# Performance work log

Measured on AMD Instinct MI355X. Metric: run time of the kernel, lower is better.

Reference implementation:

```python
import jax, jax.numpy as jnp
import numpy as np

TEMPERATURE = 1.0
NEG = -1e9
EPS = 1e-8


def setup_inputs() -> dict:
    key = jax.random.key(0)
    k1, k2, k3 = jax.random.split(key, 3)
    B, H = 524288, 32
    scores = jax.random.normal(k1, (B, H), dtype=jnp.float32)
    rankings = jax.random.randint(k2, (B, H), 0, 33, dtype=jnp.int32)
    mask = jax.random.randint(k3, (B, H), 0, 2, dtype=jnp.int32).astype(bool)
    return {"scores": scores, "rankings": rankings, "mask": mask}


def reference(scores, rankings, mask):
    B, H = scores.shape
    # effective validity: horse present AND has a ranking > 0 (top_k=None)
    m = mask & (rankings > 0)
    # masked, temperature-scaled scores; -1e9 entries underflow to exactly 0 in softmax
    s = jnp.where(m, scores / TEMPERATURE, NEG)
    p = jax.nn.softmax(s, axis=1)  # [B, H], ~0 at invalid slots

    n_valid = jnp.sum(m, axis=1)  # [B]
    # ideal order: valid horses sorted by ranking ascending (invalid pushed to end)
    rank_key = jnp.where(m, rankings, jnp.iinfo(jnp.int32).max)
    rank_order = jnp.argsort(rank_key, axis=1)          # stable sort
    # prediction order: valid horses in original index order (matches torch.where)
    pos_order = jnp.argsort(~m, axis=1)                 # stable: valid first

    q = jnp.take_along_axis(p, rank_order, axis=1)      # ideal_probs, aligned by list position
    pr = jnp.take_along_axis(p, pos_order, axis=1)      # pred_probs,  aligned by list position

    # positions >= n_valid are padding
    valid_pos = jnp.arange(H)[None, :] < n_valid[:, None]
    q_safe = jnp.where(valid_pos, q, 1.0)
    pr_safe = jnp.where(valid_pos, pr, 1.0)
    # KL(ideal || pred) with the original's log(pred + 1e-8)
    kl_terms = q_safe * (jnp.log(q_safe) - jnp.log(pr_safe + EPS))
    kl = jnp.sum(jnp.where(valid_pos, kl_terms, 0.0), axis=1)  # [B]

    # rows with <= 1 valid ranked horse are skipped entirely
    row_ok = n_valid > 1
    n_rows = jnp.maximum(jnp.sum(row_ok), 1)
    return jnp.sum(jnp.where(row_ok, kl, 0.0)) / n_rows  # reduction='mean'
```

## Files before the change

kernel.cpp:

```cpp
#include <hip/hip_runtime.h>
#include <stdint.h>


#define H 32
#define BLK 256
#define WPB 4
#define ROWD 17
#define WREGION (64 * ROWD)

__global__ __launch_bounds__(BLK) void listwise_kernel(
    const float* __restrict__ scores,
    const int* __restrict__ rankings,
    const unsigned char* __restrict__ mask_u8,
    float* __restrict__ part_kl,
    float* __restrict__ part_cnt,
    int nrows)
{
    __shared__ uint32_t stage[WPB * WREGION];
    __shared__ float s_kl[WPB], s_cnt[WPB];

    const int tid  = threadIdx.x;
    const int lane = tid & 63;
    const int wid  = tid >> 6;
    uint32_t* wbuf = &stage[wid * WREGION];
    const int wrow0 = blockIdx.x * BLK + wid * 64;

    float kl = 0.0f, cnt = 0.0f;
    uint32_t kp[16], sw[16];
    int nv = 0;
    bool have_row = false;
    unsigned short* rowp = (unsigned short*)&wbuf[lane * ROWD];

    const bool full = (wrow0 + 64 <= nrows);

    uint4 pr[8], ps[8];
    uint32_t pmw[8];
    if (full) {
        const uint4* r4 = (const uint4*)(rankings + (size_t)wrow0 * H);
        const uint4* s4 = (const uint4*)(scores + (size_t)wrow0 * H);
        const uint32_t* m1 = (const uint32_t*)(mask_u8 + (size_t)wrow0 * H);
        #pragma unroll
        for (int c = 0; c < 8; ++c) pr[c] = r4[lane + 64 * c];
        #pragma unroll
        for (int c = 0; c < 8; ++c) ps[c] = s4[lane + 64 * c];
        #pragma unroll
        for (int c = 0; c < 8; ++c) pmw[c] = m1[lane + 64 * c];
    }

    unsigned char probe = mask_u8[lane];
    const bool mask_is_i32 =
        (__ballot(((lane & 3) != 0) && (probe != 0)) == 0ull);

    if (full) {
        have_row = true;

        #pragma unroll
        for (int c = 0; c < 8; ++c) {
            const uint4 v = ps[c];
            const int L = (lane + 64 * c) << 2;
            uint32_t* d = &wbuf[(L >> 5) * ROWD + ((L & 31) >> 1)];
            d[0] = ((v.x + 0x8000u) >> 16) | (((v.y + 0x8000u) >> 16) << 16);
            d[1] = ((v.z + 0x8000u) >> 16) | (((v.w + 0x8000u) >> 16) << 16);
        }
        {
            const uint32_t* rb = &wbuf[lane * ROWD];
            #pragma unroll
            for (int a = 0; a < 16; ++a) sw[a] = rb[a];
        }

        if (!mask_is_i32) {
            #pragma unroll
            for (int c = 0; c < 8; ++c) {
                const uint4 rv = pr[c];
                const uint32_t mv = pmw[c];
                const int L = (lane + 64 * c) << 2;
                const uint32_t t0 = ((mv & 0x000000FFu) != 0u && (int)rv.x > 0) ? (rv.x << 5) : 0x4000u;
                const uint32_t t1 = ((mv & 0x0000FF00u) != 0u && (int)rv.y > 0) ? (rv.y << 5) : 0x4000u;
                const uint32_t t2 = ((mv & 0x00FF0000u) != 0u && (int)rv.z > 0) ? (rv.z << 5) : 0x4000u;
                const uint32_t t3 = ((mv & 0xFF000000u) != 0u && (int)rv.w > 0) ? (rv.w << 5) : 0x4000u;
                uint32_t* d = &wbuf[(L >> 5) * ROWD + ((L & 31) >> 1)];
                d[0] = t0 | (t1 << 16);
                d[1] = t2 | (t3 << 16);
            }
        } else {
            const uint4* m4 =
                (const uint4*)((const uint32_t*)mask_u8 + (size_t)wrow0 * H);
            #pragma unroll
            for (int c = 0; c < 8; ++c) {
                const uint4 rv = pr[c];
                const uint4 mv = m4[lane + 64 * c];
                const int L = (lane + 64 * c) << 2;
                const uint32_t t0 = (mv.x != 0u && (int)rv.x > 0) ? (rv.x << 5) : 0x4000u;
                const uint32_t t1 = (mv.y != 0u && (int)rv.y > 0) ? (rv.y << 5) : 0x4000u;
                const uint32_t t2 = (mv.z != 0u && (int)rv.z > 0) ? (rv.z << 5) : 0x4000u;
                const uint32_t t3 = (mv.w != 0u && (int)rv.w > 0) ? (rv.w << 5) : 0x4000u;
                uint32_t* d = &wbuf[(L >> 5) * ROWD + ((L & 31) >> 1)];
                d[0] = t0 | (t1 << 16);
                d[1] = t2 | (t3 << 16);
            }
        }
        {
            const uint32_t* rb = &wbuf[lane * ROWD];
            uint32_t inv2 = 0;
            #pragma unroll
            for (int a = 0; a < 16; ++a) {
                const uint32_t w = rb[a];
                kp[a] = w | ((uint32_t)(2 * a) | (((uint32_t)(2 * a + 1)) << 16));
                inv2 += (w >> 14) & 0x00010001u;
            }
            nv = 32 - (int)((inv2 & 0xFFFFu) + (inv2 >> 16));
        }
        {
            int jp = 0;
            #pragma unroll
            for (int a = 0; a < 16; ++a) {
                const uint32_t s2 = sw[a];
                const uint32_t kw = kp[a];
                const bool v0 = (kw & 0xFFFFu) < 0x4000u;
                const bool v1 = (kw >> 16) < 0x4000u;
                rowp[v0 ? jp : 33] = (unsigned short)(s2 & 0xFFFFu);
                jp += v0 ? 1 : 0;
                rowp[v1 ? jp : 33] = (unsigned short)(s2 >> 16);
                jp += v1 ? 1 : 0;
            }
        }
    } else if (wrow0 + lane < nrows) {
        have_row = true;
        const int row = wrow0 + lane;
        const int*   rptr = rankings + (size_t)row * H;
        const float* sptr = scores + (size_t)row * H;
        uint32_t vbits = 0;
        if (mask_is_i32) {
            const int* mp = (const int*)mask_u8 + (size_t)row * H;
            #pragma unroll
            for (int k = 0; k < H; ++k) vbits |= (mp[k] != 0 ? 1u : 0u) << k;
        } else {
            const unsigned char* mp = mask_u8 + (size_t)row * H;
            #pragma unroll
            for (int k = 0; k < H; ++k) vbits |= (mp[k] != 0 ? 1u : 0u) << k;
        }
        int jp = 0;
        #pragma unroll
        for (int a = 0; a < 16; ++a) {
            uint32_t kq[2], bq[2];
            #pragma unroll
            for (int q = 0; q < 2; ++q) {
                const int k = 2 * a + q;
                const int r = rptr[k];
                const bool valid = (((vbits >> k) & 1u) != 0u) && (r > 0);
                kq[q] = valid ? ((((uint32_t)r) << 5) | (uint32_t)k)
                              : (0x4000u | (uint32_t)k);
                nv += valid ? 1 : 0;
                bq[q] = (__float_as_uint(sptr[k]) + 0x8000u) >> 16;
                rowp[valid ? jp : 33] = (unsigned short)bq[q];
                jp += valid ? 1 : 0;
            }
            kp[a] = kq[0] | (kq[1] << 16);
            sw[a] = bq[0] | (bq[1] << 16);
        }
    }

    if (have_row) {
        uint32_t w32[32];
        #pragma unroll
        for (int a = 0; a < 16; ++a) {
            const uint32_t kw = kp[a], s2 = sw[a];
            w32[2 * a]     = (kw << 16) | (s2 & 0xFFFFu);
            w32[2 * a + 1] = (kw & 0xFFFF0000u) | (s2 >> 16);
        }
        #pragma unroll
        for (int k = 2; k <= 32; k <<= 1) {
            #pragma unroll
            for (int j = k >> 1; j > 0; j >>= 1) {
                #pragma unroll
                for (int i = 0; i < 32; ++i) {
                    const int l = i ^ j;
                    if (l > i) {
                        const uint32_t a = w32[i], b = w32[l];
                        const uint32_t mn = a < b ? a : b;
                        const uint32_t mx = a < b ? b : a;
                        const bool up = ((i & k) == 0);
                        w32[i] = up ? mn : mx;
                        w32[l] = up ? mx : mn;
                    }
                }
            }
        }

        float se = 0.0f, num = 0.0f;
        const uint32_t* rbd = &wbuf[lane * ROWD];
        #pragma unroll
        for (int a = 0; a < 16; ++a) {
            const uint32_t cw = rbd[a];
            #pragma unroll
            for (int q = 0; q < 2; ++q) {
                const uint32_t wv = w32[2 * a + q];
                const bool valid = wv < 0x40000000u;
                const float s_i = __uint_as_float(wv << 16);
                const uint32_t c16 = q ? (cw >> 16) : (cw & 0xFFFFu);
                const float g = __uint_as_float(c16 << 16);
                float e = __expf(s_i);
                e = valid ? e : 0.0f;
                const float d2 = valid ? (s_i - g) : 0.0f;
                se += e;
                num = __builtin_fmaf(e, d2, num);
            }
        }
        if (nv > 1) { kl = __fdividef(num, se); cnt = 1.0f; }
    }

    #pragma unroll
    for (int m = 32; m >= 1; m >>= 1) {
        kl  += __shfl_xor(kl, m);
        cnt += __shfl_xor(cnt, m);
    }
    if (lane == 0) { s_kl[wid] = kl; s_cnt[wid] = cnt; }
    __syncthreads();
    if (tid == 0) {
        part_kl[blockIdx.x]  = s_kl[0] + s_kl[1] + s_kl[2] + s_kl[3];
        part_cnt[blockIdx.x] = s_cnt[0] + s_cnt[1] + s_cnt[2] + s_cnt[3];
    }
}

__global__ __launch_bounds__(256) void finalize_kernel(
    const float* __restrict__ part_kl,
    const float* __restrict__ part_cnt,
    float* __restrict__ out, int nblk)
{
    float k = 0.0f, c = 0.0f;
    for (int i = threadIdx.x; i < nblk; i += 256) {
        k += part_kl[i];
        c += part_cnt[i];
    }
    #pragma unroll
    for (int m = 32; m >= 1; m >>= 1) {
        k += __shfl_xor(k, m);
        c += __shfl_xor(c, m);
    }
    __shared__ float sk[4], sc[4];
    const int wid = threadIdx.x >> 6;
    if ((threadIdx.x & 63) == 0) { sk[wid] = k; sc[wid] = c; }
    __syncthreads();
    if (threadIdx.x == 0) {
        float K = sk[0] + sk[1] + sk[2] + sk[3];
        float C = sc[0] + sc[1] + sc[2] + sc[3];
        if (C < 1.0f) C = 1.0f;
        out[0] = K / C;
    }
}

extern "C" void kernel_launch(void* const* d_in, const int* in_sizes, int n_in,
                              void* d_out, int out_size, void* d_ws, size_t ws_size,
                              hipStream_t stream) {
    const float* scores = (const float*)d_in[0];
    const int* rankings = (const int*)d_in[1];
    const unsigned char* mask = (const unsigned char*)d_in[2];
    float* out = (float*)d_out;

    const int total = in_sizes[0];
    const int nrows = total / H;
    const int blocks = (nrows + BLK - 1) / BLK;

    float* part_kl  = (float*)d_ws;
    float* part_cnt = (float*)d_ws + blocks;

    listwise_kernel<<<blocks, BLK, 0, stream>>>(
        scores, rankings, mask, part_kl, part_cnt, nrows);

    finalize_kernel<<<1, 256, 0, stream>>>(part_kl, part_cnt, out, blocks);
}
```

Baseline: 199.7 us.

## Rewrite as persistent single-wave blocks with double-buffered global-to-LDS loads

Replaces the 256-thread blocks with 64-thread persistent blocks (about 1024 of them), each looping over several 64-row tiles. Rankings, scores and the u8 mask are copied straight into LDS with global_load_lds, double-buffered so the next tile's load overlaps compute on the current one. Instead of compacting valid scores through LDS, each row now builds two key arrays and sorts both with a bitonic network: one ordered by ranking, one by original index. This is meant to hide memory latency and cut LDS round trips, at the cost of a second sort per row, fewer waves in flight, and a full vmcnt(0) wait per tile.

```diff
diff --git a/kernel.cpp b/kernel.cpp
--- a/kernel.cpp
+++ b/kernel.cpp
@@ -3,210 +3,225 @@
 
 
 #define H 32
-#define BLK 256
-#define WPB 4
-#define ROWD 17
-#define WREGION (64 * ROWD)
-
-__global__ __launch_bounds__(BLK) void listwise_kernel(
+#define TPB 64
+#define RANK_DW 2048
+#define SCORE_DW 2048
+#define MASK_DW 512
+#define BUF_DW (RANK_DW + SCORE_DW + MASK_DW)
+
+__device__ __forceinline__ void glds16(const void* g, void* l) {
+    __builtin_amdgcn_global_load_lds(
+        (const __attribute__((address_space(1))) void*)g,
+        (__attribute__((address_space(3))) void*)l, 16, 0, 0);
+}
+
+__device__ __forceinline__ void sort32(uint32_t* w) {
+    #pragma unroll
+    for (int k = 2; k <= 32; k <<= 1) {
+        #pragma unroll
+        for (int j = k >> 1; j > 0; j >>= 1) {
+            #pragma unroll
+            for (int i = 0; i < 32; ++i) {
+                const int l = i ^ j;
+                if (l > i) {
+                    const uint32_t a = w[i], b = w[l];
+                    const uint32_t mn = a < b ? a : b;
+                    const uint32_t mx = a < b ? b : a;
+                    const bool up = ((i & k) == 0);
+                    w[i] = up ? mn : mx;
+                    w[l] = up ? mx : mn;
+                }
+            }
+        }
+    }
+}
+
+__global__ __launch_bounds__(TPB) void listwise_kernel(
     const float* __restrict__ scores,
     const int* __restrict__ rankings,
     const unsigned char* __restrict__ mask_u8,
     float* __restrict__ part_kl,
     float* __restrict__ part_cnt,
-    int nrows)
+    int nrows, int tpw)
 {
-    __shared__ uint32_t stage[WPB * WREGION];
-    __shared__ float s_kl[WPB], s_cnt[WPB];
-
-    const int tid  = threadIdx.x;
-    const int lane = tid & 63;
-    const int wid  = tid >> 6;
-    uint32_t* wbuf = &stage[wid * WREGION];
-    const int wrow0 = blockIdx.x * BLK + wid * 64;
-
-    float kl = 0.0f, cnt = 0.0f;
-    uint32_t kp[16], sw[16];
-    int nv = 0;
-    bool have_row = false;
-    unsigned short* rowp = (unsigned short*)&wbuf[lane * ROWD];
-
-    const bool full = (wrow0 + 64 <= nrows);
-
-    uint4 pr[8], ps[8];
-    uint32_t pmw[8];
-    if (full) {
-        const uint4* r4 = (const uint4*)(rankings + (size_t)wrow0 * H);
-        const uint4* s4 = (const uint4*)(scores + (size_t)wrow0 * H);
-        const uint32_t* m1 = (const uint32_t*)(mask_u8 + (size_t)wrow0 * H);
-        #pragma unroll
-        for (int c = 0; c < 8; ++c) pr[c] = r4[lane + 64 * c];
-        #pragma unroll
-        for (int c = 0; c < 8; ++c) ps[c] = s4[lane + 64 * c];
-        #pragma unroll
-        for (int c = 0; c < 8; ++c) pmw[c] = m1[lane + 64 * c];
-    }
+    __shared__ __align__(16) uint32_t buf[2][BUF_DW];
+
+    const int lane  = threadIdx.x;
+    const int tile0 = blockIdx.x * tpw;
 
     unsigned char probe = mask_u8[lane];
+    {
+        const int r0 = tile0 * 64;
+        if (r0 + 64 <= nrows) {
+            const char* rb = (const char*)(rankings + (size_t)r0 * H);
+            const char* sb = (const char*)(scores + (size_t)r0 * H);
+            #pragma unroll
+            for (int c = 0; c < 8; ++c)
+                glds16(rb + c * 1024 + lane * 16, &buf[0][c * 256]);
+            #pragma unroll
+            for (int c = 0; c < 8; ++c)
+                glds16(sb + c * 1024 + lane * 16, &buf[0][RANK_DW + c * 256]);
+        }
+    }
     const bool mask_is_i32 =
         (__ballot(((lane & 3) != 0) && (probe != 0)) == 0ull);
-
-    if (full) {
-        have_row = true;
-
-        #pragma unroll
-        for (int c = 0; c < 8; ++c) {
-            const uint4 v = ps[c];
-            const int L = (lane + 64 * c) << 2;
-            uint32_t* d = &wbuf[(L >> 5) * ROWD + ((L & 31) >> 1)];
-            d[0] = ((v.x + 0x8000u) >> 16) | (((v.y + 0x8000u) >> 16) << 16);
-            d[1] = ((v.z + 0x8000u) >> 16) | (((v.w + 0x8000u) >> 16) << 16);
-        }
+    {
+        const int r0 = tile0 * 64;
+        if (!mask_is_i32 && r0 + 64 <= nrows) {
+            const char* mb = (const char*)(mask_u8 + (size_t)r0 * H);
+            #pragma unroll
+            for (int c = 0; c < 2; ++c)
+                glds16(mb + c * 1024 + lane * 16,
+                       &buf[0][RANK_DW + SCORE_DW + c * 256]);
+        }
+    }
+
+    float kl = 0.0f, cnt = 0.0f;
+    int cur = 0;
+
+    for (int tt = 0; tt < tpw; ++tt) {
+        const int row0 = (tile0 + tt) * 64;
+        if (row0 >= nrows) break;
+        const bool full = (row0 + 64 <= nrows);
+
+        if (full) {
+            asm volatile("s_waitcnt vmcnt(0)" ::: "memory");
+            __builtin_amdgcn_sched_barrier(0);
+        }
+
         {
-            const uint32_t* rb = &wbuf[lane * ROWD];
-            #pragma unroll
-            for (int a = 0; a < 16; ++a) sw[a] = rb[a];
-        }
-
-        if (!mask_is_i32) {
-            #pragma unroll
-            for (int c = 0; c < 8; ++c) {
-                const uint4 rv = pr[c];
-                const uint32_t mv = pmw[c];
-                const int L = (lane + 64 * c) << 2;
-                const uint32_t t0 = ((mv & 0x000000FFu) != 0u && (int)rv.x > 0) ? (rv.x << 5) : 0x4000u;
-                const uint32_t t1 = ((mv & 0x0000FF00u) != 0u && (int)rv.y > 0) ? (rv.y << 5) : 0x4000u;
-                const uint32_t t2 = ((mv & 0x00FF0000u) != 0u && (int)rv.z > 0) ? (rv.z << 5) : 0x4000u;
-                const uint32_t t3 = ((mv & 0xFF000000u) != 0u && (int)rv.w > 0) ? (rv.w << 5) : 0x4000u;
-                uint32_t* d = &wbuf[(L >> 5) * ROWD + ((L & 31) >> 1)];
-                d[0] = t0 | (t1 << 16);
-                d[1] = t2 | (t3 << 16);
-            }
-        } else {
-            const uint4* m4 =
-                (const uint4*)((const uint32_t*)mask_u8 + (size_t)wrow0 * H);
-            #pragma unroll
-            for (int c = 0; c < 8; ++c) {
-                const uint4 rv = pr[c];
-                const uint4 mv = m4[lane + 64 * c];
-                const int L = (lane + 64 * c) << 2;
-                const uint32_t t0 = (mv.x != 0u && (int)rv.x > 0) ? (rv.x << 5) : 0x4000u;
-                const uint32_t t1 = (mv.y != 0u && (int)rv.y > 0) ? (rv.y << 5) : 0x4000u;
-                const uint32_t t2 = (mv.z != 0u && (int)rv.z > 0) ? (rv.z << 5) : 0x4000u;
-                const uint32_t t3 = (mv.w != 0u && (int)rv.w > 0) ? (rv.w << 5) : 0x4000u;
-                uint32_t* d = &wbuf[(L >> 5) * ROWD + ((L & 31) >> 1)];
-                d[0] = t0 | (t1 << 16);
-                d[1] = t2 | (t3 << 16);
-            }
-        }
-        {
-            const uint32_t* rb = &wbuf[lane * ROWD];
-            uint32_t inv2 = 0;
-            #pragma unroll
-            for (int a = 0; a < 16; ++a) {
-                const uint32_t w = rb[a];
-                kp[a] = w | ((uint32_t)(2 * a) | (((uint32_t)(2 * a + 1)) << 16));
-                inv2 += (w >> 14) & 0x00010001u;
-            }
-            nv = 32 - (int)((inv2 & 0xFFFFu) + (inv2 >> 16));
-        }
-        {
-            int jp = 0;
-            #pragma unroll
-            for (int a = 0; a < 16; ++a) {
-                const uint32_t s2 = sw[a];
-                const uint32_t kw = kp[a];
-                const bool v0 = (kw & 0xFFFFu) < 0x4000u;
-                const bool v1 = (kw >> 16) < 0x4000u;
-                rowp[v0 ? jp : 33] = (unsigned short)(s2 & 0xFFFFu);
-                jp += v0 ? 1 : 0;
-                rowp[v1 ? jp : 33] = (unsigned short)(s2 >> 16);
-                jp += v1 ? 1 : 0;
-            }
-        }
-    } else if (wrow0 + lane < nrows) {
-        have_row = true;
-        const int row = wrow0 + lane;
-        const int*   rptr = rankings + (size_t)row * H;
-        const float* sptr = scores + (size_t)row * H;
-        uint32_t vbits = 0;
-        if (mask_is_i32) {
-            const int* mp = (const int*)mask_u8 + (size_t)row * H;
-            #pragma unroll
-            for (int k = 0; k < H; ++k) vbits |= (mp[k] != 0 ? 1u : 0u) << k;
-        } else {
-            const unsigned char* mp = mask_u8 + (size_t)row * H;
-            #pragma unroll
-            for (int k = 0; k < H; ++k) vbits |= (mp[k] != 0 ? 1u : 0u) << k;
-        }
-        int jp = 0;
-        #pragma unroll
-        for (int a = 0; a < 16; ++a) {
-            uint32_t kq[2], bq[2];
-            #pragma unroll
-            for (int q = 0; q < 2; ++q) {
-                const int k = 2 * a + q;
-                const int r = rptr[k];
-                const bool valid = (((vbits >> k) & 1u) != 0u) && (r > 0);
-                kq[q] = valid ? ((((uint32_t)r) << 5) | (uint32_t)k)
-                              : (0x4000u | (uint32_t)k);
-                nv += valid ? 1 : 0;
-                bq[q] = (__float_as_uint(sptr[k]) + 0x8000u) >> 16;
-                rowp[valid ? jp : 33] = (unsigned short)bq[q];
-                jp += valid ? 1 : 0;
-            }
-            kp[a] = kq[0] | (kq[1] << 16);
-            sw[a] = bq[0] | (bq[1] << 16);
-        }
-    }
-
-    if (have_row) {
-        uint32_t w32[32];
-        #pragma unroll
-        for (int a = 0; a < 16; ++a) {
-            const uint32_t kw = kp[a], s2 = sw[a];
-            w32[2 * a]     = (kw << 16) | (s2 & 0xFFFFu);
-            w32[2 * a + 1] = (kw & 0xFFFF0000u) | (s2 >> 16);
-        }
-        #pragma unroll
-        for (int k = 2; k <= 32; k <<= 1) {
-            #pragma unroll
-            for (int j = k >> 1; j > 0; j >>= 1) {
-                #pragma unroll
-                for (int i = 0; i < 32; ++i) {
-                    const int l = i ^ j;
-                    if (l > i) {
-                        const uint32_t a = w32[i], b = w32[l];
-                        const uint32_t mn = a < b ? a : b;
-                        const uint32_t mx = a < b ? b : a;
-                        const bool up = ((i & k) == 0);
-                        w32[i] = up ? mn : mx;
-                        w32[l] = up ? mx : mn;
-                    }
-                }
-            }
-        }
-
-        float se = 0.0f, num = 0.0f;
-        const uint32_t* rbd = &wbuf[lane * ROWD];
-        #pragma unroll
-        for (int a = 0; a < 16; ++a) {
-            const uint32_t cw = rbd[a];
-            #pragma unroll
-            for (int q = 0; q < 2; ++q) {
-                const uint32_t wv = w32[2 * a + q];
-                const bool valid = wv < 0x40000000u;
-                const float s_i = __uint_as_float(wv << 16);
-                const uint32_t c16 = q ? (cw >> 16) : (cw & 0xFFFFu);
-                const float g = __uint_as_float(c16 << 16);
+            const int nr0 = row0 + 64;
+            if (tt + 1 < tpw && nr0 + 64 <= nrows) {
+                const int nb = cur ^ 1;
+                const char* rb = (const char*)(rankings + (size_t)nr0 * H);
+                const char* sb = (const char*)(scores + (size_t)nr0 * H);
+                #pragma unroll
+                for (int c = 0; c < 8; ++c)
+                    glds16(rb + c * 1024 + lane * 16, &buf[nb][c * 256]);
+                #pragma unroll
+                for (int c = 0; c < 8; ++c)
+                    glds16(sb + c * 1024 + lane * 16,
+                           &buf[nb][RANK_DW + c * 256]);
+                if (!mask_is_i32) {
+                    const char* mb = (const char*)(mask_u8 + (size_t)nr0 * H);
+                    #pragma unroll
+                    for (int c = 0; c < 2; ++c)
+                        glds16(mb + c * 1024 + lane * 16,
+                               &buf[nb][RANK_DW + SCORE_DW + c * 256]);
+                }
+            }
+        }
+
+        uint32_t w1[32], w2[32];
+        int nv = 0;
+        bool do_row = false;
+
+        if (full) {
+            do_row = true;
+            const uint32_t* rrow = &buf[cur][0] + lane * 32;
+            const uint32_t* srow = &buf[cur][RANK_DW] + lane * 32;
+            const uint32_t* mrow = &buf[cur][RANK_DW + SCORE_DW] + lane * 8;
+
+            uint32_t vbits = 0;
+            if (!mask_is_i32) {
+                #pragma unroll
+                for (int j = 0; j < 8; ++j) {
+                    const int slot = (j + lane) & 7;
+                    uint32_t m = mrow[slot];
+                    uint32_t t2 = m | (m >> 1); t2 |= t2 >> 2; t2 |= t2 >> 4;
+                    uint32_t nib = ((t2 & 0x01010101u) * 0x01020408u) >> 24;
+                    vbits |= (nib & 0xFu) << (4 * slot);
+                }
+            } else {
+                const uint4* mp = (const uint4*)
+                    ((const uint32_t*)mask_u8 + (size_t)(row0 + lane) * H);
+                #pragma unroll
+                for (int c = 0; c < 8; ++c) {
+                    const uint4 v = mp[c];
+                    vbits |= (v.x ? 1u : 0u) << (4 * c)
+                           | (v.y ? 1u : 0u) << (4 * c + 1)
+                           | (v.z ? 1u : 0u) << (4 * c + 2)
+                           | (v.w ? 1u : 0u) << (4 * c + 3);
+                }
+            }
+
+            #pragma unroll
+            for (int p = 0; p < 16; ++p) {
+                const int slot = (p + lane) & 15;
+                const uint2 rr = *(const uint2*)(rrow + 2 * slot);
+                const uint2 ss = *(const uint2*)(srow + 2 * slot);
+                const uint32_t k0 = 2 * slot, k1 = 2 * slot + 1;
+                const uint32_t b0 = (ss.x + 0x8000u) >> 16;
+                const uint32_t b1 = (ss.y + 0x8000u) >> 16;
+                const bool v0 = ((vbits >> k0) & 1u) && ((int)rr.x > 0);
+                const bool v1 = ((vbits >> k1) & 1u) && ((int)rr.y > 0);
+                const uint32_t k1a = v0 ? ((rr.x << 5) | k0) : (0x4000u | k0);
+                const uint32_t k1b = v1 ? ((rr.y << 5) | k1) : (0x4000u | k1);
+                const uint32_t k2a = v0 ? k0 : (0x4000u | k0);
+                const uint32_t k2b = v1 ? k1 : (0x4000u | k1);
+                w1[2 * p]     = (k1a << 16) | b0;
+                w1[2 * p + 1] = (k1b << 16) | b1;
+                w2[2 * p]     = (k2a << 16) | b0;
+                w2[2 * p + 1] = (k2b << 16) | b1;
+                nv += (v0 ? 1 : 0) + (v1 ? 1 : 0);
+            }
+        } else if (row0 + lane < nrows) {
+            do_row = true;
+            const int row = row0 + lane;
+            const uint2* rp2 = (const uint2*)(rankings + (size_t)row * H);
+            const uint2* sp2 = (const uint2*)(scores + (size_t)row * H);
+            uint32_t vbits = 0;
+            if (mask_is_i32) {
+                const int* mp = (const int*)mask_u8 + (size_t)row * H;
+                #pragma unroll
+                for (int k = 0; k < H; ++k)
+                    vbits |= (mp[k] != 0 ? 1u : 0u) << k;
+            } else {
+                const unsigned char* mp = mask_u8 + (size_t)row * H;
+                #pragma unroll
+                for (int k = 0; k < H; ++k)
+                    vbits |= (mp[k] != 0 ? 1u : 0u) << k;
+            }
+            #pragma unroll
+            for (int p = 0; p < 16; ++p) {
+                const uint2 rr = rp2[p];
+                const uint2 ss = sp2[p];
+                const uint32_t k0 = 2 * p, k1 = 2 * p + 1;
+                const uint32_t b0 = (ss.x + 0x8000u) >> 16;
+                const uint32_t b1 = (ss.y + 0x8000u) >> 16;
+                const bool v0 = ((vbits >> k0) & 1u) && ((int)rr.x > 0);
+                const bool v1 = ((vbits >> k1) & 1u) && ((int)rr.y > 0);
+                const uint32_t k1a = v0 ? ((rr.x << 5) | k0) : (0x4000u | k0);
+                const uint32_t k1b = v1 ? ((rr.y << 5) | k1) : (0x4000u | k1);
+                const uint32_t k2a = v0 ? k0 : (0x4000u | k0);
+                const uint32_t k2b = v1 ? k1 : (0x4000u | k1);
+                w1[2 * p]     = (k1a << 16) | b0;
+                w1[2 * p + 1] = (k1b << 16) | b1;
+                w2[2 * p]     = (k2a << 16) | b0;
+                w2[2 * p + 1] = (k2b << 16) | b1;
+                nv += (v0 ? 1 : 0) + (v1 ? 1 : 0);
+            }
+        }
+
+        if (do_row) {
+            sort32(w1);
+            sort32(w2);
+            float se = 0.0f, num = 0.0f;
+            #pragma unroll
+            for (int i = 0; i < 32; ++i) {
+                const uint32_t a = w1[i], c = w2[i];
+                const bool valid = a < 0x40000000u;
+                const float s_i = __uint_as_float(a << 16);
+                const float g   = __uint_as_float(c << 16);
                 float e = __expf(s_i);
                 e = valid ? e : 0.0f;
                 const float d2 = valid ? (s_i - g) : 0.0f;
                 se += e;
                 num = __builtin_fmaf(e, d2, num);
             }
-        }
-        if (nv > 1) { kl = __fdividef(num, se); cnt = 1.0f; }
+            if (nv > 1) { kl += __fdividef(num, se); cnt += 1.0f; }
+        }
+        cur ^= 1;
     }
 
     #pragma unroll
@@ -214,11 +229,9 @@
         kl  += __shfl_xor(kl, m);
         cnt += __shfl_xor(cnt, m);
     }
-    if (lane == 0) { s_kl[wid] = kl; s_cnt[wid] = cnt; }
-    __syncthreads();
-    if (tid == 0) {
-        part_kl[blockIdx.x]  = s_kl[0] + s_kl[1] + s_kl[2] + s_kl[3];
-        part_cnt[blockIdx.x] = s_cnt[0] + s_cnt[1] + s_cnt[2] + s_cnt[3];
+    if (lane == 0) {
+        part_kl[blockIdx.x]  = kl;
+        part_cnt[blockIdx.x] = cnt;
     }
 }
 
@@ -259,13 +272,16 @@
 
     const int total = in_sizes[0];
     const int nrows = total / H;
-    const int blocks = (nrows + BLK - 1) / BLK;
+    const int total_tiles = (nrows + 63) / 64;
+    int tpw = (total_tiles + 1023) / 1024;
+    if (tpw < 1) tpw = 1;
+    const int blocks = (total_tiles + tpw - 1) / tpw;
 
     float* part_kl  = (float*)d_ws;
     float* part_cnt = (float*)d_ws + blocks;
 
-    listwise_kernel<<<blocks, BLK, 0, stream>>>(
-        scores, rankings, mask, part_kl, part_cnt, nrows);
+    listwise_kernel<<<blocks, TPB, 0, stream>>>(
+        scores, rankings, mask, part_kl, part_cnt, nrows, tpw);
 
     finalize_kernel<<<1, 256, 0, stream>>>(part_kl, part_cnt, out, blocks);
 }
```

After: 210.6 us. +5.5%, slower.
